# Kernel tuning notes

Hardware: AMD Instinct MI355X
Metric: run time of the kernel (lower is better)

The kernel has to match this reference:

```python
import jax, jax.numpy as jnp
import numpy as np

B, L = 256, 50            # batch, n_pos (session length)
ITEM_DIM, POS_DIM = 128, 64
DIM = ITEM_DIM + POS_DIM  # 192
N_ITEMS = 50000
W = 20.0                  # temperature / init scale
LN_EPS = 1e-5


def renorm(t, max_norm=1.5):
    # torch Embedding max_norm semantics: clip row L2 norm to max_norm
    n = jnp.linalg.norm(t, axis=-1, keepdims=True)
    return t * jnp.minimum(1.0, max_norm / jnp.maximum(n, 1e-7))


def setup_inputs() -> dict:
    key = jax.random.key(0)
    ks = jax.random.split(key, 24)
    inv_w = 1.0 / W
    lb = 1.0 / np.sqrt(DIM)
    lb3 = 1.0 / np.sqrt(3 * DIM)
    u = lambda k, shape, b: jax.random.uniform(k, shape, jnp.float32, -b, b)
    emb = jax.random.normal(ks[0], (N_ITEMS, ITEM_DIM), jnp.float32).at[0].set(0.0)
    pos_emb = jax.random.normal(ks[1], (L + 1, POS_DIM), jnp.float32).at[0].set(0.0)
    return {
        'x': jax.random.randint(ks[20], (B, L), 0, N_ITEMS),
        'pos': jnp.sort(jax.random.randint(ks[21], (B, L), 1, L + 1), axis=-1),
        'emb': emb,
        'pos_emb': pos_emb,
        'vw0': jax.random.normal(ks[2], (1, DIM), jnp.float32) * inv_w,
        'vw1': jax.random.normal(ks[3], (DIM, DIM), jnp.float32) * inv_w,
        'vw2': jax.random.normal(ks[4], (DIM, DIM), jnp.float32) * inv_w,
        'vbias': jnp.zeros((DIM,), jnp.float32),
        'w1_W': u(ks[5], (DIM, DIM), lb), 'w1_b': u(ks[6], (DIM,), lb),
        'w2_W': u(ks[7], (DIM, DIM), lb), 'w2_b': u(ks[8], (DIM,), lb),
        'wA': jax.random.normal(ks[9], (1, L), jnp.float32) * inv_w,
        'wg1_W': u(ks[10], (DIM, DIM), lb), 'wg1_b': u(ks[11], (DIM,), lb),
        'wg2_W': u(ks[12], (DIM, DIM), lb), 'wg2_b': u(ks[13], (DIM,), lb),
        'gq': jax.random.normal(ks[14], (DIM, 1), jnp.float32) * inv_w,
        'wf_W': u(ks[15], (ITEM_DIM, 3 * DIM), lb3), 'wf_b': u(ks[16], (ITEM_DIM,), lb3),
        'ln_g': jnp.ones((DIM,), jnp.float32), 'ln_b': jnp.zeros((DIM,), jnp.float32),
    }


def reference(x, pos, emb, pos_emb, vw0, vw1, vw2, vbias, w1_W, w1_b, w2_W, w2_b,
              wA, wg1_W, wg1_b, wg2_W, wg2_b, gq, wf_W, wf_b, ln_g, ln_b):
    emb_r = renorm(emb)
    x_e = emb_r[x]                                   # [B,L,item_dim]
    p_e = renorm(pos_emb)[pos]                       # [B,L,pos_dim]
    x_ = jnp.concatenate([x_e, p_e], axis=-1)        # [B,L,D]
    mask = (x != 0)                                  # [B,L]

    # --- vanila (additive) attention, all n_pos targets in one fused pass ---
    K = x_ @ vw1                                     # [B,L,D]  (shared across targets)
    Q = x_ @ vw2                                     # [B,L,D]
    h = jax.nn.relu(K[:, None, :, :] + Q[:, :, None, :] + vbias)   # [B,Li,Lj,D]
    alpha = jnp.einsum('bijd,d->bij', h, vw0[0])     # scores over keys j
    alpha = jnp.where(mask[:, None, :], alpha, -jnp.inf)
    a = jax.nn.softmax(alpha, axis=-1)
    S = jnp.einsum('bij,bjd->bid', a, x_)            # [B,L,D]

    # --- MLP + LayerNorm + position mixing ---
    h2 = jax.nn.relu(S @ w1_W.T + w1_b)
    S2 = h2 @ w2_W.T + w2_b + S
    mu = jnp.mean(S2, axis=-1, keepdims=True)
    var = jnp.mean((S2 - mu) ** 2, axis=-1, keepdims=True)
    S3 = ln_g * (S2 - mu) * jax.lax.rsqrt(var + LN_EPS) + ln_b
    st = jnp.einsum('p,bpd->bd', wA[0], S3)[:, None, :]   # [B,1,D]

    # --- global attention ---
    sl = x_[:, -1:, :]                               # [B,1,D]
    g = jax.nn.sigmoid(x_ @ wg1_W.T + wg1_b + (sl @ wg2_W.T + wg2_b))
    ag = g @ gq                                      # [B,L,1]
    sg = jnp.einsum('blo,bld->bod', ag, x_)          # [B,1,D]

    # --- decoder: cosine-similarity logits against item embeddings ---
    c = jax.nn.selu(jnp.concatenate([st, sl, sg], axis=-1) @ wf_W.T + wf_b)[:, 0, :]
    c = c / jnp.linalg.norm(c, axis=-1, keepdims=True)
    le = emb_r[1:]
    le = le / jnp.linalg.norm(le, axis=-1, keepdims=True)
    z = W * (c @ le.T)                               # [B, n_items-1]
    return z
```

## Files before the change

kernel.cpp:

```cpp
#include <hip/hip_runtime.h>
#include <hip/hip_bf16.h>
#include <math.h>
#include <stdint.h>

#define BB 256
#define LL 50
#define IDIM 128
#define PDIM 64
#define DIM 192
#define NITEMS 50000
#define NOUT 49999
#define WSC 20.0f
#define EPS 1e-5f
#define WMAT (DIM * DIM)

typedef __attribute__((ext_vector_type(8))) short  short8;
typedef __attribute__((ext_vector_type(4))) float  f32x4;

__device__ __forceinline__ unsigned short f2bf(float f) {
    unsigned int u = __float_as_uint(f);
    u = (u + 0x7FFFu + ((u >> 16) & 1u)) >> 16;
    return (unsigned short)u;
}

__global__ __launch_bounds__(256) void k_norms(const float* __restrict__ emb,
                                               float* __restrict__ scale,
                                               float* __restrict__ invn,
                                               unsigned short* __restrict__ emb16) {
    int row  = blockIdx.x * 4 + (threadIdx.x >> 6);
    int lane = threadIdx.x & 63;
    const float* p = emb + (size_t)row * IDIM;
    float a = p[lane], b = p[lane + 64];
    emb16[(size_t)row * IDIM + lane]      = f2bf(a);
    emb16[(size_t)row * IDIM + lane + 64] = f2bf(b);
    float s = a * a + b * b;
#pragma unroll
    for (int off = 32; off; off >>= 1) s += __shfl_xor(s, off);
    if (lane == 0) {
        float n = sqrtf(s);
        scale[row] = fminf(1.0f, 1.5f / fmaxf(n, 1e-7f));
        invn[row]  = (n > 0.f) ? 1.f / n : 0.f;
    }
}

__global__ __launch_bounds__(64) void k_pnorms(const float* __restrict__ pe,
                                               float* __restrict__ pscale) {
    int row = threadIdx.x;
    if (row > LL) return;
    float s = 0.f;
    const float* p = pe + row * PDIM;
    for (int d = 0; d < PDIM; ++d) { float v = p[d]; s += v * v; }
    float n = sqrtf(s);
    pscale[row] = fminf(1.0f, 1.5f / fmaxf(n, 1e-7f));
}

__global__ __launch_bounds__(256) void k_cvtw(const float* __restrict__ vw1, const float* __restrict__ vw2,
                                              const float* __restrict__ w1W, const float* __restrict__ w2W,
                                              const float* __restrict__ wg1W,
                                              unsigned short* __restrict__ Wout) {
    int b = blockIdx.x;
    int wi = b / 144;
    int pos = (b % 144) * 256 + threadIdx.x;
    int n = pos / DIM, k = pos - n * DIM;
    float v;
    if      (wi == 0) v = vw1[(size_t)k * DIM + n];
    else if (wi == 1) v = vw2[(size_t)k * DIM + n];
    else if (wi == 2) v = w1W[pos];
    else if (wi == 3) v = w2W[pos];
    else              v = wg1W[pos];
    Wout[(size_t)wi * WMAT + pos] = f2bf(v);
}

__global__ __launch_bounds__(512) void k_mega(
    const int* __restrict__ x, const int* __restrict__ pos,
    const float* __restrict__ emb, const float* __restrict__ pe,
    const float* __restrict__ scale, const float* __restrict__ pscale,
    const unsigned short* __restrict__ W16,
    const float* __restrict__ vw0, const float* __restrict__ vbias,
    const float* __restrict__ w1b, const float* __restrict__ w2b,
    const float* __restrict__ wg1b, const float* __restrict__ wg2W,
    const float* __restrict__ wg2b, const float* __restrict__ gq,
    const float* __restrict__ wA, const float* __restrict__ lng,
    const float* __restrict__ lnb, const float* __restrict__ wfW,
    const float* __restrict__ wfb, unsigned short* __restrict__ Cb16g) {

    __shared__ float Xs[LL * DIM];
    __shared__ unsigned short Bs16[64 * DIM];
    __shared__ float R1[LL * 196];
    __shared__ float R2[LL * 196];
    __shared__ float GLs[DIM];
    __shared__ float cvec[3 * DIM];
    __shared__ float ags[64];
    __shared__ int   msk[64];
    __shared__ float was[64];
    __shared__ float red[8];
    __shared__ int   xi[LL], pii[LL];
    __shared__ float xsc[LL], psc[LL];

    const int b = blockIdx.x, t = threadIdx.x;
    const int wv = t >> 6, l = t & 63;
    const int lr = l & 15, lk = l >> 4;

    if (t < LL) {
        int v = x[b * LL + t];  xi[t] = v;  xsc[t] = scale[v];
        int pv = pos[b * LL + t]; pii[t] = pv; psc[t] = pscale[pv];
    }
    if (t >= 64 && t < 128) ags[t - 64] = 0.f;
    if (t >= 128 && t < 128 + LL) was[t - 128] = wA[t - 128];
    __syncthreads();
    if (t < 64) msk[t] = (t < LL) ? xi[t] : 0;
    for (int e = t; e < LL * DIM; e += 512) {
        int r = e / DIM, d = e - r * DIM;
        float v;
        if (d < IDIM) v = emb[(size_t)xi[r] * IDIM + d] * xsc[r];
        else          v = pe[pii[r] * PDIM + (d - IDIM)] * psc[r];
        Xs[e] = v;
        int byte = r * 384 + d * 2; byte ^= (r & 7) << 4;
        *(unsigned short*)((char*)Bs16 + byte) = f2bf(v);
    }
    for (int e = t; e < 14 * DIM; e += 512) Bs16[LL * DIM + ((50 * DIM - LL * DIM) ? 0 : 0) + e] = 0;
    __syncthreads();

    if (t < DIM) {
        float g = wg2b[t];
        const float* wr = wg2W + (size_t)t * DIM;
        float s0 = 0, s1 = 0, s2 = 0, s3 = 0;
        const float* xr = &Xs[49 * DIM];
        for (int k = 0; k < DIM; k += 4) {
            float4 w4 = *(const float4*)(wr + k);
            s0 += xr[k] * w4.x; s1 += xr[k + 1] * w4.y; s2 += xr[k + 2] * w4.z; s3 += xr[k + 3] * w4.w;
        }
        GLs[t] = g + ((s0 + s1) + (s2 + s3));
    }
    __syncthreads();

    {
        short8 afr[4][6];
#pragma unroll
        for (int mt = 0; mt < 4; ++mt) {
            int row = mt * 16 + lr;
#pragma unroll
            for (int ks = 0; ks < 6; ++ks) {
                int byte = row * 384 + (lk * 8 + ks * 32) * 2; byte ^= (row & 7) << 4;
                afr[mt][ks] = *(const short8*)((const char*)Bs16 + byte);
            }
        }
        for (int task = wv; task < 36; task += 8) {
            int out = task / 12, nt = task % 12;
            int ncol = nt * 16 + lr;
            const unsigned short* bp = W16 + (size_t)(out == 0 ? 0 : (out == 1 ? 1 : 4)) * WMAT
                                       + (size_t)ncol * DIM + lk * 8;
            f32x4 a0 = {}, a1 = {}, a2 = {}, a3 = {};
#pragma unroll
            for (int ks = 0; ks < 6; ++ks) {
                short8 bf = *(const short8*)(bp + ks * 32);
                a0 = __builtin_amdgcn_mfma_f32_16x16x32_bf16(afr[0][ks], bf, a0, 0, 0, 0);
                a1 = __builtin_amdgcn_mfma_f32_16x16x32_bf16(afr[1][ks], bf, a1, 0, 0, 0);
                a2 = __builtin_amdgcn_mfma_f32_16x16x32_bf16(afr[2][ks], bf, a2, 0, 0, 0);
                a3 = __builtin_amdgcn_mfma_f32_16x16x32_bf16(afr[3][ks], bf, a3, 0, 0, 0);
            }
            if (out == 0) {
                float bia = vbias[ncol];
#pragma unroll
                for (int mt = 0; mt < 4; ++mt) {
                    f32x4 ac = (mt == 0) ? a0 : (mt == 1) ? a1 : (mt == 2) ? a2 : a3;
#pragma unroll
                    for (int r = 0; r < 4; ++r) {
                        int gr = mt * 16 + lk * 4 + r;
                        if (gr < LL) R1[gr * 196 + ncol] = ac[r] + bia;
                    }
                }
            } else if (out == 1) {
#pragma unroll
                for (int mt = 0; mt < 4; ++mt) {
                    f32x4 ac = (mt == 0) ? a0 : (mt == 1) ? a1 : (mt == 2) ? a2 : a3;
#pragma unroll
                    for (int r = 0; r < 4; ++r) {
                        int gr = mt * 16 + lk * 4 + r;
                        if (gr < LL) R2[gr * 196 + ncol] = ac[r];
                    }
                }
            } else {
                float bia = wg1b[ncol] + GLs[ncol];
                float gqv = gq[ncol];
#pragma unroll
                for (int mt = 0; mt < 4; ++mt) {
                    f32x4 ac = (mt == 0) ? a0 : (mt == 1) ? a1 : (mt == 2) ? a2 : a3;
                    float c0, c1, c2, c3;
                    {
                        int gr0 = mt * 16 + lk * 4;
                        float v0 = ac[0] + bia, v1 = ac[1] + bia, v2 = ac[2] + bia, v3 = ac[3] + bia;
                        c0 = (gr0 + 0 < LL) ? gqv / (1.f + expf(-v0)) : 0.f;
                        c1 = (gr0 + 1 < LL) ? gqv / (1.f + expf(-v1)) : 0.f;
                        c2 = (gr0 + 2 < LL) ? gqv / (1.f + expf(-v2)) : 0.f;
                        c3 = (gr0 + 3 < LL) ? gqv / (1.f + expf(-v3)) : 0.f;
                    }
#pragma unroll
                    for (int off = 1; off < 16; off <<= 1) {
                        c0 += __shfl_xor(c0, off); c1 += __shfl_xor(c1, off);
                        c2 += __shfl_xor(c2, off); c3 += __shfl_xor(c3, off);
                    }
                    if (lr == 0) {
                        int gr0 = mt * 16 + lk * 4;
                        if (gr0 + 0 < LL) atomicAdd(&ags[gr0 + 0], c0);
                        if (gr0 + 1 < LL) atomicAdd(&ags[gr0 + 1], c1);
                        if (gr0 + 2 < LL) atomicAdd(&ags[gr0 + 2], c2);
                        if (gr0 + 3 < LL) atomicAdd(&ags[gr0 + 3], c3);
                    }
                }
            }
        }
    }
    __syncthreads();

    {
        const int d0 = wv * 24;
        float kr[24], wr[24];
        {
            const float* wp = vw0 + d0;
#pragma unroll
            for (int q = 0; q < 6; ++q) {
                float4 v = *(const float4*)(wp + q * 4);
                wr[q * 4] = v.x; wr[q * 4 + 1] = v.y; wr[q * 4 + 2] = v.z; wr[q * 4 + 3] = v.w;
            }
            if (l < LL) {
                const float* kp = R1 + l * 196 + d0;
#pragma unroll
                for (int q = 0; q < 6; ++q) {
                    float4 v = *(const float4*)(kp + q * 4);
                    kr[q * 4] = v.x; kr[q * 4 + 1] = v.y; kr[q * 4 + 2] = v.z; kr[q * 4 + 3] = v.w;
                }
            } else {
#pragma unroll
                for (int q = 0; q < 24; ++q) kr[q] = 0.f;
            }
        }
        __syncthreads();
        float* parts = R1;
        float* Ab    = R1 + 6144;
        const float NEG = -__builtin_inff();
        bool valid = (l < LL) && (msk[l] != 0);
        for (int i0 = 0; i0 < LL; i0 += 12) {
            int cnt = (i0 + 12 <= LL) ? 12 : (LL - i0);
            for (int i = 0; i < cnt; ++i) {
                const float* qrow = R2 + (i0 + i) * 196 + d0;
                float b0 = 0, b1 = 0, b2 = 0, b3 = 0;
#pragma unroll
                for (int q = 0; q < 6; ++q) {
                    float4 qv = *(const float4*)(qrow + q * 4);
                    b0 += fmaxf(kr[q * 4 + 0] + qv.x, 0.f) * wr[q * 4 + 0];
                    b1 += fmaxf(kr[q * 4 + 1] + qv.y, 0.f) * wr[q * 4 + 1];
                    b2 += fmaxf(kr[q * 4 + 2] + qv.z, 0.f) * wr[q * 4 + 2];
                    b3 += fmaxf(kr[q * 4 + 3] + qv.w, 0.f) * wr[q * 4 + 3];
                }
                parts[(wv * 12 + i) * 64 + l] = (b0 + b1) + (b2 + b3);
            }
            __syncthreads();
            for (int i = wv; i < cnt; i += 8) {
                float aj = 0.f;
#pragma unroll
                for (int w2 = 0; w2 < 8; ++w2) aj += parts[(w2 * 12 + i) * 64 + l];
                if (!valid) aj = NEG;
                float m = aj;
#pragma unroll
                for (int off = 32; off; off >>= 1) m = fmaxf(m, __shfl_xor(m, off));
                float e = valid ? expf(aj - m) : 0.f;
                float s = e;
#pragma unroll
                for (int off = 32; off; off >>= 1) s += __shfl_xor(s, off);
                Ab[(i0 + i) * 64 + l] = e / s;
            }
            __syncthreads();
        }
    }

    {
        const float* Ab = R1 + 6144;
        for (int o = t; o < LL * DIM; o += 512) {
            int i = o / DIM, d = o - i * DIM;
            float s = 0.f;
#pragma unroll
            for (int q = 0; q < 12; ++q) {
                float4 av = *(const float4*)(Ab + i * 64 + q * 4);
                s += av.x * Xs[(q * 4 + 0) * DIM + d] + av.y * Xs[(q * 4 + 1) * DIM + d]
                   + av.z * Xs[(q * 4 + 2) * DIM + d] + av.w * Xs[(q * 4 + 3) * DIM + d];
            }
            s += Ab[i * 64 + 48] * Xs[48 * DIM + d] + Ab[i * 64 + 49] * Xs[49 * DIM + d];
            R2[i * 196 + d] = s;
            int byte = i * 384 + d * 2; byte ^= (i & 7) << 4;
            *(unsigned short*)((char*)Bs16 + byte) = f2bf(s);
        }
    }
    __syncthreads();

    {
        short8 sfr[4][6];
#pragma unroll
        for (int mt = 0; mt < 4; ++mt) {
            int row = mt * 16 + lr;
#pragma unroll
            for (int ks = 0; ks < 6; ++ks) {
                int byte = row * 384 + (lk * 8 + ks * 32) * 2; byte ^= (row & 7) << 4;
                sfr[mt][ks] = *(const short8*)((const char*)Bs16 + byte);
            }
        }
        f32x4 h0[4] = {}, h1[4] = {};
        {
            int ncol = wv * 16 + lr;
            const unsigned short* bp = W16 + (size_t)2 * WMAT + (size_t)ncol * DIM + lk * 8;
#pragma unroll
            for (int ks = 0; ks < 6; ++ks) {
                short8 bf = *(const short8*)(bp + ks * 32);
                h0[0] = __builtin_amdgcn_mfma_f32_16x16x32_bf16(sfr[0][ks], bf, h0[0], 0, 0, 0);
                h0[1] = __builtin_amdgcn_mfma_f32_16x16x32_bf16(sfr[1][ks], bf, h0[1], 0, 0, 0);
                h0[2] = __builtin_amdgcn_mfma_f32_16x16x32_bf16(sfr[2][ks], bf, h0[2], 0, 0, 0);
                h0[3] = __builtin_amdgcn_mfma_f32_16x16x32_bf16(sfr[3][ks], bf, h0[3], 0, 0, 0);
            }
        }
        if (wv < 4) {
            int ncol = (wv + 8) * 16 + lr;
            const unsigned short* bp = W16 + (size_t)2 * WMAT + (size_t)ncol * DIM + lk * 8;
#pragma unroll
            for (int ks = 0; ks < 6; ++ks) {
                short8 bf = *(const short8*)(bp + ks * 32);
                h1[0] = __builtin_amdgcn_mfma_f32_16x16x32_bf16(sfr[0][ks], bf, h1[0], 0, 0, 0);
                h1[1] = __builtin_amdgcn_mfma_f32_16x16x32_bf16(sfr[1][ks], bf, h1[1], 0, 0, 0);
                h1[2] = __builtin_amdgcn_mfma_f32_16x16x32_bf16(sfr[2][ks], bf, h1[2], 0, 0, 0);
                h1[3] = __builtin_amdgcn_mfma_f32_16x16x32_bf16(sfr[3][ks], bf, h1[3], 0, 0, 0);
            }
        }
        __syncthreads();
        {
            int gc = wv * 16 + lr;
            float bia = w1b[gc];
#pragma unroll
            for (int mt = 0; mt < 4; ++mt)
#pragma unroll
                for (int r = 0; r < 4; ++r) {
                    int gr = mt * 16 + lk * 4 + r;
                    if (gr < LL) {
                        float v = fmaxf(h0[mt][r] + bia, 0.f);
                        int byte = gr * 384 + gc * 2; byte ^= (gr & 7) << 4;
                        *(unsigned short*)((char*)Bs16 + byte) = f2bf(v);
                    }
                }
        }
        if (wv < 4) {
            int gc = (wv + 8) * 16 + lr;
            float bia = w1b[gc];
#pragma unroll
            for (int mt = 0; mt < 4; ++mt)
#pragma unroll
                for (int r = 0; r < 4; ++r) {
                    int gr = mt * 16 + lk * 4 + r;
                    if (gr < LL) {
                        float v = fmaxf(h1[mt][r] + bia, 0.f);
                        int byte = gr * 384 + gc * 2; byte ^= (gr & 7) << 4;
                        *(unsigned short*)((char*)Bs16 + byte) = f2bf(v);
                    }
                }
        }
    }
    __syncthreads();

    {
        short8 hfr[4][6];
#pragma unroll
        for (int mt = 0; mt < 4; ++mt) {
            int row = mt * 16 + lr;
#pragma unroll
            for (int ks = 0; ks < 6; ++ks) {
                int byte = row * 384 + (lk * 8 + ks * 32) * 2; byte ^= (row & 7) << 4;
                hfr[mt][ks] = *(const short8*)((const char*)Bs16 + byte);
            }
        }
        for (int nt = wv; nt < 12; nt += 8) {
            int ncol = nt * 16 + lr;
            const unsigned short* bp = W16 + (size_t)3 * WMAT + (size_t)ncol * DIM + lk * 8;
            f32x4 s0 = {}, s1 = {}, s2 = {}, s3 = {};
#pragma unroll
            for (int ks = 0; ks < 6; ++ks) {
                short8 bf = *(const short8*)(bp + ks * 32);
                s0 = __builtin_amdgcn_mfma_f32_16x16x32_bf16(hfr[0][ks], bf, s0, 0, 0, 0);
                s1 = __builtin_amdgcn_mfma_f32_16x16x32_bf16(hfr[1][ks], bf, s1, 0, 0, 0);
                s2 = __builtin_amdgcn_mfma_f32_16x16x32_bf16(hfr[2][ks], bf, s2, 0, 0, 0);
                s3 = __builtin_amdgcn_mfma_f32_16x16x32_bf16(hfr[3][ks], bf, s3, 0, 0, 0);
            }
            float bia = w2b[ncol];
#pragma unroll
            for (int mt = 0; mt < 4; ++mt) {
                f32x4 ac = (mt == 0) ? s0 : (mt == 1) ? s1 : (mt == 2) ? s2 : s3;
#pragma unroll
                for (int r = 0; r < 4; ++r) {
                    int gr = mt * 16 + lk * 4 + r;
                    if (gr < LL) R2[gr * 196 + ncol] = ac[r] + bia + R2[gr * 196 + ncol];
                }
            }
        }
    }
    __syncthreads();

    for (int r = wv; r < LL; r += 8) {
        float* p = R2 + r * 196;
        float v0 = p[l], v1 = p[l + 64], v2 = p[l + 128];
        float s = v0 + v1 + v2;
#pragma unroll
        for (int off = 32; off; off >>= 1) s += __shfl_xor(s, off);
        float mu = s * (1.f / DIM);
        float d0 = v0 - mu, d1 = v1 - mu, d2 = v2 - mu;
        float q = d0 * d0 + d1 * d1 + d2 * d2;
#pragma unroll
        for (int off = 32; off; off >>= 1) q += __shfl_xor(q, off);
        float inv = rsqrtf(q * (1.f / DIM) + EPS);
        p[l]       = lng[l] * d0 * inv + lnb[l];
        p[l + 64]  = lng[l + 64] * d1 * inv + lnb[l + 64];
        p[l + 128] = lng[l + 128] * d2 * inv + lnb[l + 128];
    }
    __syncthreads();

    if (t < DIM) {
        float st = 0.f;
        for (int p = 0; p < LL; ++p) st += was[p] * R2[p * 196 + t];
        cvec[t] = st;
        cvec[DIM + t] = Xs[49 * DIM + t];
        float sg = 0.f;
        for (int lr2 = 0; lr2 < LL; ++lr2) sg += ags[lr2] * Xs[lr2 * DIM + t];
        cvec[2 * DIM + t] = sg;
    }
    __syncthreads();

    float cj = 0.f;
    if (t < IDIM) {
        float s = wfb[t];
        const float* wr = wfW + (size_t)t * (3 * DIM);
        for (int e = 0; e < 3 * DIM; e += 4) {
            float4 w4 = *(const float4*)(wr + e);
            s += cvec[e] * w4.x + cvec[e + 1] * w4.y + cvec[e + 2] * w4.z + cvec[e + 3] * w4.w;
        }
        const float sa = 1.6732632423543772f, sc = 1.0507009873554805f;
        cj = sc * (s > 0.f ? s : sa * expm1f(s));
    }
    float sq = cj * cj;
#pragma unroll
    for (int off = 32; off; off >>= 1) sq += __shfl_xor(sq, off);
    if (l == 0) red[wv] = sq;
    __syncthreads();
    if (t < IDIM) {
        float nrm = sqrtf(red[0] + red[1]);
        Cb16g[b * IDIM + t] = f2bf(cj / nrm);
    }
}

__global__ __launch_bounds__(256) void k_z4(const unsigned short* __restrict__ Cb16,
                                            const unsigned short* __restrict__ emb16,
                                            const float* __restrict__ invn,
                                            float* __restrict__ Z) {
    __shared__ float tr[4][64][68];
    int n0 = blockIdx.x * 64;
    int t = threadIdx.x, w = t >> 6, l = t & 63;
    int lr = l & 15, lk = l >> 4;

    short8 a[4][4];
#pragma unroll
    for (int mt = 0; mt < 4; ++mt) {
        int mrow = w * 64 + mt * 16 + lr;
        const unsigned short* ap = Cb16 + (size_t)mrow * IDIM + lk * 8;
#pragma unroll
        for (int ks = 0; ks < 4; ++ks) a[mt][ks] = *(const short8*)(ap + ks * 32);
    }
    f32x4 acc[4][4] = {};
#pragma unroll
    for (int nt = 0; nt < 4; ++nt) {
        int nrow = n0 + nt * 16 + lr;
        short8 bfr[4];
        if (nrow < NOUT) {
            const unsigned short* bp = emb16 + (size_t)(nrow + 1) * IDIM + lk * 8;
#pragma unroll
            for (int ks = 0; ks < 4; ++ks) bfr[ks] = *(const short8*)(bp + ks * 32);
        } else {
            short8 z = {};
#pragma unroll
            for (int ks = 0; ks < 4; ++ks) bfr[ks] = z;
        }
#pragma unroll
        for (int mt = 0; mt < 4; ++mt)
#pragma unroll
            for (int ks = 0; ks < 4; ++ks)
                acc[mt][nt] = __builtin_amdgcn_mfma_f32_16x16x32_bf16(a[mt][ks], bfr[ks], acc[mt][nt], 0, 0, 0);
    }
#pragma unroll
    for (int nt = 0; nt < 4; ++nt) {
        int gn = n0 + nt * 16 + lr;
        float sc = (gn < NOUT) ? WSC * invn[gn + 1] : 0.f;
#pragma unroll
        for (int mt = 0; mt < 4; ++mt)
#pragma unroll
            for (int r = 0; r < 4; ++r)
                tr[w][mt * 16 + lk * 4 + r][nt * 16 + lr] = acc[mt][nt][r] * sc;
    }
    __syncthreads();
    int q = l >> 4, s = l & 15;
    bool tail = (n0 + 64) > NOUT;
#pragma unroll
    for (int it = 0; it < 16; ++it) {
        int row = it * 4 + q;
        int gm  = w * 64 + row;
        float4 v = *(const float4*)&tr[w][row][s * 4];
        if (!tail) {
            *(float4*)&Z[(size_t)gm * NOUT + n0 + s * 4] = v;
        } else {
            int c0 = n0 + s * 4;
            float vv[4] = {v.x, v.y, v.z, v.w};
#pragma unroll
            for (int j = 0; j < 4; ++j)
                if (c0 + j < NOUT) Z[(size_t)gm * NOUT + c0 + j] = vv[j];
        }
    }
}

extern "C" void kernel_launch(void* const* d_in, const int* in_sizes, int n_in,
                              void* d_out, int out_size, void* d_ws, size_t ws_size,
                              hipStream_t stream) {
    const int*   x     = (const int*)d_in[0];
    const int*   pos   = (const int*)d_in[1];
    const float* emb   = (const float*)d_in[2];
    const float* pose  = (const float*)d_in[3];
    const float* vw0   = (const float*)d_in[4];
    const float* vw1   = (const float*)d_in[5];
    const float* vw2   = (const float*)d_in[6];
    const float* vbias = (const float*)d_in[7];
    const float* w1W   = (const float*)d_in[8];
    const float* w1b   = (const float*)d_in[9];
    const float* w2W   = (const float*)d_in[10];
    const float* w2b   = (const float*)d_in[11];
    const float* wA    = (const float*)d_in[12];
    const float* wg1W  = (const float*)d_in[13];
    const float* wg1b  = (const float*)d_in[14];
    const float* wg2W  = (const float*)d_in[15];
    const float* wg2b  = (const float*)d_in[16];
    const float* gq    = (const float*)d_in[17];
    const float* wfW   = (const float*)d_in[18];
    const float* wfb   = (const float*)d_in[19];
    const float* lng   = (const float*)d_in[20];
    const float* lnb   = (const float*)d_in[21];
    float* Z = (float*)d_out;

    float* w = (float*)d_ws;
    float* scale  = w; w += NITEMS;
    float* invn   = w; w += NITEMS;
    float* pscale = w; w += 64;
    w = (float*)(((uintptr_t)w + 15) & ~(uintptr_t)15);
    unsigned short* emb16 = (unsigned short*)w; w += (size_t)NITEMS * IDIM / 2;
    unsigned short* W16   = (unsigned short*)w; w += (size_t)5 * WMAT / 2;
    unsigned short* Cb16  = (unsigned short*)w; w += (size_t)BB * IDIM / 2;

    k_norms<<<NITEMS / 4, 256, 0, stream>>>(emb, scale, invn, emb16);
    k_pnorms<<<1, 64, 0, stream>>>(pose, pscale);
    k_cvtw<<<5 * 144, 256, 0, stream>>>(vw1, vw2, w1W, w2W, wg1W, W16);
    k_mega<<<BB, 512, 0, stream>>>(x, pos, emb, pose, scale, pscale, W16,
                                   vw0, vbias, w1b, w2b, wg1b, wg2W, wg2b, gq,
                                   wA, lng, lnb, wfW, wfb, Cb16);
    k_z4<<<(NOUT + 63) / 64, 256, 0, stream>>>(Cb16, emb16, invn, Z);
}
```

Measured before the change: 124.7 us.

## Use MFMA for attention-weighted sum and split decoder matvec across threads

Replaces the scalar fp32 a@X attention-weighted sum with bf16 MFMA tiles. It stores a transposed bf16 copy of X and bf16 softmax weights in shared memory and drops the fp32 Xs buffer. It also spreads the final 576-wide decoder matvec over all 512 threads with a partial-sum reduction, and moves the global-attention sum onto a separate group of threads. This cuts scalar FLOPs and LDS traffic in k_mega at the cost of extra bf16 rounding of the attention weights and X.

Result: faster. 109.9 us (-11.8%).

```diff
diff --git a/kernel.cpp b/kernel.cpp
--- a/kernel.cpp
+++ b/kernel.cpp
@@ -21,6 +21,10 @@
     unsigned int u = __float_as_uint(f);
     u = (u + 0x7FFFu + ((u >> 16) & 1u)) >> 16;
     return (unsigned short)u;
+}
+__device__ __forceinline__ float bf2f(unsigned short u) {
+    unsigned int v = ((unsigned int)u) << 16;
+    return __uint_as_float(v);
 }
 
 __global__ __launch_bounds__(256) void k_norms(const float* __restrict__ emb,
@@ -84,12 +88,15 @@
     const float* __restrict__ lnb, const float* __restrict__ wfW,
     const float* __restrict__ wfb, unsigned short* __restrict__ Cb16g) {
 
-    __shared__ float Xs[LL * DIM];
     __shared__ unsigned short Bs16[64 * DIM];
+    __shared__ unsigned short X16T[DIM * 72];
+    __shared__ unsigned short Ab16[64 * 72];
     __shared__ float R1[LL * 196];
     __shared__ float R2[LL * 196];
+    __shared__ float xlast[DIM];
     __shared__ float GLs[DIM];
     __shared__ float cvec[3 * DIM];
+    __shared__ float red2[4][128];
     __shared__ float ags[64];
     __shared__ int   msk[64];
     __shared__ float was[64];
@@ -109,26 +116,33 @@
     if (t >= 128 && t < 128 + LL) was[t - 128] = wA[t - 128];
     __syncthreads();
     if (t < 64) msk[t] = (t < LL) ? xi[t] : 0;
-    for (int e = t; e < LL * DIM; e += 512) {
-        int r = e / DIM, d = e - r * DIM;
-        float v;
-        if (d < IDIM) v = emb[(size_t)xi[r] * IDIM + d] * xsc[r];
-        else          v = pe[pii[r] * PDIM + (d - IDIM)] * psc[r];
-        Xs[e] = v;
-        int byte = r * 384 + d * 2; byte ^= (r & 7) << 4;
-        *(unsigned short*)((char*)Bs16 + byte) = f2bf(v);
-    }
-    for (int e = t; e < 14 * DIM; e += 512) Bs16[LL * DIM + ((50 * DIM - LL * DIM) ? 0 : 0) + e] = 0;
+    for (int r = wv; r < LL; r += 8) {
+        float sx = xsc[r], sp = psc[r];
+        float v0 = emb[(size_t)xi[r] * IDIM + l] * sx;
+        float v1 = emb[(size_t)xi[r] * IDIM + l + 64] * sx;
+        float v2 = pe[pii[r] * PDIM + l] * sp;
+        int base = r * 384, sw = (r & 7) << 4;
+        *(unsigned short*)((char*)Bs16 + ((base + l * 2) ^ sw))         = f2bf(v0);
+        *(unsigned short*)((char*)Bs16 + ((base + (l + 64) * 2) ^ sw))  = f2bf(v1);
+        *(unsigned short*)((char*)Bs16 + ((base + (l + 128) * 2) ^ sw)) = f2bf(v2);
+        X16T[l * 72 + r]         = f2bf(v0);
+        X16T[(l + 64) * 72 + r]  = f2bf(v1);
+        X16T[(l + 128) * 72 + r] = f2bf(v2);
+        if (r == 49) { xlast[l] = v0; xlast[l + 64] = v1; xlast[l + 128] = v2; }
+    }
+    for (int e = t; e < 14 * DIM; e += 512) Bs16[LL * DIM + e] = 0;
+    for (int e = t; e < DIM * 14; e += 512) { int d = e / 14, j = 50 + (e - d * 14); X16T[d * 72 + j] = 0; }
+    for (int e = t; e < 14 * 72; e += 512) Ab16[50 * 72 + e] = 0;
     __syncthreads();
 
     if (t < DIM) {
         float g = wg2b[t];
         const float* wr = wg2W + (size_t)t * DIM;
         float s0 = 0, s1 = 0, s2 = 0, s3 = 0;
-        const float* xr = &Xs[49 * DIM];
         for (int k = 0; k < DIM; k += 4) {
             float4 w4 = *(const float4*)(wr + k);
-            s0 += xr[k] * w4.x; s1 += xr[k + 1] * w4.y; s2 += xr[k + 2] * w4.z; s3 += xr[k + 3] * w4.w;
+            s0 += xlast[k] * w4.x; s1 += xlast[k + 1] * w4.y;
+            s2 += xlast[k + 2] * w4.z; s3 += xlast[k + 3] * w4.w;
         }
         GLs[t] = g + ((s0 + s1) + (s2 + s3));
     }
@@ -141,7 +155,7 @@
             int row = mt * 16 + lr;
 #pragma unroll
             for (int ks = 0; ks < 6; ++ks) {
-                int byte = row * 384 + (lk * 8 + ks * 32) * 2; byte ^= (row & 7) << 4;
+                int byte = (row * 384 + (lk * 8 + ks * 32) * 2) ^ ((row & 7) << 4);
                 afr[mt][ks] = *(const short8*)((const char*)Bs16 + byte);
             }
         }
@@ -186,22 +200,18 @@
 #pragma unroll
                 for (int mt = 0; mt < 4; ++mt) {
                     f32x4 ac = (mt == 0) ? a0 : (mt == 1) ? a1 : (mt == 2) ? a2 : a3;
-                    float c0, c1, c2, c3;
-                    {
-                        int gr0 = mt * 16 + lk * 4;
-                        float v0 = ac[0] + bia, v1 = ac[1] + bia, v2 = ac[2] + bia, v3 = ac[3] + bia;
-                        c0 = (gr0 + 0 < LL) ? gqv / (1.f + expf(-v0)) : 0.f;
-                        c1 = (gr0 + 1 < LL) ? gqv / (1.f + expf(-v1)) : 0.f;
-                        c2 = (gr0 + 2 < LL) ? gqv / (1.f + expf(-v2)) : 0.f;
-                        c3 = (gr0 + 3 < LL) ? gqv / (1.f + expf(-v3)) : 0.f;
-                    }
+                    int gr0 = mt * 16 + lk * 4;
+                    float v0 = ac[0] + bia, v1 = ac[1] + bia, v2 = ac[2] + bia, v3 = ac[3] + bia;
+                    float c0 = (gr0 + 0 < LL) ? gqv / (1.f + expf(-v0)) : 0.f;
+                    float c1 = (gr0 + 1 < LL) ? gqv / (1.f + expf(-v1)) : 0.f;
+                    float c2 = (gr0 + 2 < LL) ? gqv / (1.f + expf(-v2)) : 0.f;
+                    float c3 = (gr0 + 3 < LL) ? gqv / (1.f + expf(-v3)) : 0.f;
 #pragma unroll
                     for (int off = 1; off < 16; off <<= 1) {
                         c0 += __shfl_xor(c0, off); c1 += __shfl_xor(c1, off);
                         c2 += __shfl_xor(c2, off); c3 += __shfl_xor(c3, off);
                     }
                     if (lr == 0) {
-                        int gr0 = mt * 16 + lk * 4;
                         if (gr0 + 0 < LL) atomicAdd(&ags[gr0 + 0], c0);
                         if (gr0 + 1 < LL) atomicAdd(&ags[gr0 + 1], c1);
                         if (gr0 + 2 < LL) atomicAdd(&ags[gr0 + 2], c2);
@@ -237,7 +247,6 @@
         }
         __syncthreads();
         float* parts = R1;
-        float* Ab    = R1 + 6144;
         const float NEG = -__builtin_inff();
         bool valid = (l < LL) && (msk[l] != 0);
         for (int i0 = 0; i0 < LL; i0 += 12) {
@@ -268,27 +277,31 @@
                 float s = e;
 #pragma unroll
                 for (int off = 32; off; off >>= 1) s += __shfl_xor(s, off);
-                Ab[(i0 + i) * 64 + l] = e / s;
+                Ab16[(i0 + i) * 72 + l] = f2bf(e / s);
             }
             __syncthreads();
         }
     }
 
-    {
-        const float* Ab = R1 + 6144;
-        for (int o = t; o < LL * DIM; o += 512) {
-            int i = o / DIM, d = o - i * DIM;
-            float s = 0.f;
-#pragma unroll
-            for (int q = 0; q < 12; ++q) {
-                float4 av = *(const float4*)(Ab + i * 64 + q * 4);
-                s += av.x * Xs[(q * 4 + 0) * DIM + d] + av.y * Xs[(q * 4 + 1) * DIM + d]
-                   + av.z * Xs[(q * 4 + 2) * DIM + d] + av.w * Xs[(q * 4 + 3) * DIM + d];
-            }
-            s += Ab[i * 64 + 48] * Xs[48 * DIM + d] + Ab[i * 64 + 49] * Xs[49 * DIM + d];
-            R2[i * 196 + d] = s;
-            int byte = i * 384 + d * 2; byte ^= (i & 7) << 4;
-            *(unsigned short*)((char*)Bs16 + byte) = f2bf(s);
+    for (int task = wv; task < 48; task += 8) {
+        int mt = task / 12, nt = task - (task / 12) * 12;
+        int i0 = mt * 16, d0c = nt * 16;
+        short8 aA0 = *(const short8*)(Ab16 + (i0 + lr) * 72 + lk * 8);
+        short8 aA1 = *(const short8*)(Ab16 + (i0 + lr) * 72 + 32 + lk * 8);
+        short8 bB0 = *(const short8*)(X16T + (d0c + lr) * 72 + lk * 8);
+        short8 bB1 = *(const short8*)(X16T + (d0c + lr) * 72 + 32 + lk * 8);
+        f32x4 ac = {};
+        ac = __builtin_amdgcn_mfma_f32_16x16x32_bf16(aA0, bB0, ac, 0, 0, 0);
+        ac = __builtin_amdgcn_mfma_f32_16x16x32_bf16(aA1, bB1, ac, 0, 0, 0);
+        int d = d0c + lr;
+#pragma unroll
+        for (int r = 0; r < 4; ++r) {
+            int i = i0 + lk * 4 + r;
+            if (i < LL) {
+                R2[i * 196 + d] = ac[r];
+                int byte = (i * 384 + d * 2) ^ ((i & 7) << 4);
+                *(unsigned short*)((char*)Bs16 + byte) = f2bf(ac[r]);
+            }
         }
     }
     __syncthreads();
@@ -300,7 +313,7 @@
             int row = mt * 16 + lr;
 #pragma unroll
             for (int ks = 0; ks < 6; ++ks) {
-                int byte = row * 384 + (lk * 8 + ks * 32) * 2; byte ^= (row & 7) << 4;
+                int byte = (row * 384 + (lk * 8 + ks * 32) * 2) ^ ((row & 7) << 4);
                 sfr[mt][ks] = *(const short8*)((const char*)Bs16 + byte);
             }
         }
@@ -340,7 +353,7 @@
                     int gr = mt * 16 + lk * 4 + r;
                     if (gr < LL) {
                         float v = fmaxf(h0[mt][r] + bia, 0.f);
-                        int byte = gr * 384 + gc * 2; byte ^= (gr & 7) << 4;
+                        int byte = (gr * 384 + gc * 2) ^ ((gr & 7) << 4);
                         *(unsigned short*)((char*)Bs16 + byte) = f2bf(v);
                     }
                 }
@@ -355,7 +368,7 @@
                     int gr = mt * 16 + lk * 4 + r;
                     if (gr < LL) {
                         float v = fmaxf(h1[mt][r] + bia, 0.f);
-                        int byte = gr * 384 + gc * 2; byte ^= (gr & 7) << 4;
+                        int byte = (gr * 384 + gc * 2) ^ ((gr & 7) << 4);
                         *(unsigned short*)((char*)Bs16 + byte) = f2bf(v);
                     }
                 }
@@ -370,7 +383,7 @@
             int row = mt * 16 + lr;
 #pragma unroll
             for (int ks = 0; ks < 6; ++ks) {
-                int byte = row * 384 + (lk * 8 + ks * 32) * 2; byte ^= (row & 7) << 4;
+                int byte = (row * 384 + (lk * 8 + ks * 32) * 2) ^ ((row & 7) << 4);
                 hfr[mt][ks] = *(const short8*)((const char*)Bs16 + byte);
             }
         }
@@ -422,21 +435,31 @@
         float st = 0.f;
         for (int p = 0; p < LL; ++p) st += was[p] * R2[p * 196 + t];
         cvec[t] = st;
-        cvec[DIM + t] = Xs[49 * DIM + t];
+        cvec[DIM + t] = xlast[t];
+    } else if (t >= 320) {
+        int d = t - 320;
         float sg = 0.f;
-        for (int lr2 = 0; lr2 < LL; ++lr2) sg += ags[lr2] * Xs[lr2 * DIM + t];
-        cvec[2 * DIM + t] = sg;
-    }
-    __syncthreads();
-
+        const unsigned short* xr = X16T + d * 72;
+        for (int p = 0; p < LL; ++p) sg += ags[p] * bf2f(xr[p]);
+        cvec[2 * DIM + d] = sg;
+    }
+    __syncthreads();
+
+    {
+        int out = t & 127, part = t >> 7;
+        float s = (part == 0) ? wfb[out] : 0.f;
+        const float* wr = wfW + (size_t)out * (3 * DIM) + part * 144;
+        const float* cv = cvec + part * 144;
+        for (int e = 0; e < 144; e += 4) {
+            float4 w4 = *(const float4*)(wr + e);
+            s += cv[e] * w4.x + cv[e + 1] * w4.y + cv[e + 2] * w4.z + cv[e + 3] * w4.w;
+        }
+        red2[part][out] = s;
+    }
+    __syncthreads();
     float cj = 0.f;
     if (t < IDIM) {
-        float s = wfb[t];
-        const float* wr = wfW + (size_t)t * (3 * DIM);
-        for (int e = 0; e < 3 * DIM; e += 4) {
-            float4 w4 = *(const float4*)(wr + e);
-            s += cvec[e] * w4.x + cvec[e + 1] * w4.y + cvec[e + 2] * w4.z + cvec[e + 3] * w4.w;
-        }
+        float s = red2[0][t] + red2[1][t] + red2[2][t] + red2[3][t];
         const float sa = 1.6732632423543772f, sc = 1.0507009873554805f;
         cj = sc * (s > 0.f ? s : sa * expm1f(s));
     }
```
